# Performance work log

Hardware: AMD Instinct MI355X
Metric: run time of the kernel (lower is better)

## Reference

```python
import jax, jax.numpy as jnp
import numpy as np

K = 3  # kernel_size

def setup_inputs() -> dict:
    key = jax.random.key(0)
    k1, k2, k3 = jax.random.split(key, 3)
    B, T, G, F, O = 4, 512, 129, 96, 96
    x = jax.random.normal(k1, (B, T, G, F), dtype=jnp.float32)
    # kaiming_uniform_(a=sqrt(5)) -> bound = sqrt(6/((1+5)*fan_in)) = 1/sqrt(fan_in), fan_in = F*K
    fan_in = F * K
    wb = 1.0 / np.sqrt(fan_in)
    weight = jax.random.uniform(k2, (G, O, F, K), dtype=jnp.float32, minval=-wb, maxval=wb)
    bias = jax.random.uniform(k3, (G, O), dtype=jnp.float32, minval=-wb, maxval=wb)
    return {"x": x, "weight": weight, "bias": bias}

def reference(x, weight, bias):
    # x: [B, T, G, F]; weight: [G, O, F, K]; bias: [G, O]
    B, T, G, F = x.shape
    pad = K // 2
    xp = jnp.pad(x, ((0, 0), (pad, pad), (0, 0), (0, 0)))  # [B, T+2p, G, F]
    # gather K shifted views -> [B, T, G, F, K] (same windows as unfold with padding K//2)
    xw = jnp.stack([xp[:, k:k + T] for k in range(K)], axis=-1)
    out = jnp.einsum('btgfk,gofk->btgo', xw, weight)
    out = out + bias  # broadcast [G, O] over [B, T, G, O]
    return out
```

## Files before the change

kernel.cpp:

```cpp
#include <hip/hip_runtime.h>

typedef unsigned short ushort_t;
typedef __attribute__((ext_vector_type(8))) short short8;
typedef __attribute__((ext_vector_type(4))) float floatx4;

#define G_   129
#define F_   96
#define O_   96
#define T_   512
#define KD   288
#define LDB  296
#define SROW 40
#define SLAB (36 * SROW)

__device__ __forceinline__ unsigned f2bf(float f) {
    unsigned u = __builtin_bit_cast(unsigned, f);
    u += 0x7FFFu + ((u >> 16) & 1u);
    return u >> 16;
}
__device__ __forceinline__ unsigned pk2(float a, float b) {
    return f2bf(a) | (f2bf(b) << 16);
}

__global__ __launch_bounds__(512, 4) void conv_mfma(
    const float* __restrict__ x, const float* __restrict__ w,
    const float* __restrict__ bias, float* __restrict__ out)
{
    __shared__ __align__(16) ushort_t Wl[O_ * LDB];
    __shared__ __align__(16) ushort_t Xs[8 * SLAB];

    const int g    = blockIdx.y;
    const int m0   = blockIdx.x * 256;
    const int tid  = threadIdx.x;
    const int wave = tid >> 6;
    const int lane = tid & 63;
    const int ln   = lane & 15;
    const int q    = lane >> 4;

    const int m0r = m0 + wave * 32;
    const int b   = m0r >> 9;
    const int tb  = m0r & 511;

    const float* tp[5];
    int  laddr[5];
    bool wr[5], vld[5];
    #pragma unroll
    for (int i = 0; i < 5; ++i) {
        int task = i * 64 + lane;
        int row = task >> 3;
        int seg = task & 7;
        int tl = tb + row - 1;
        wr[i]  = row < 34;
        vld[i] = wr[i] && ((unsigned)tl < (unsigned)T_);
        int tc = tl < 0 ? 0 : (tl > T_ - 1 ? T_ - 1 : tl);
        tp[i] = x + ((size_t)((b * T_ + tc) * G_ + g) * F_ + seg * 4);
        laddr[i] = wave * SLAB + row * SROW + seg * 4;
    }

    auto issueX = [&](int fb, floatx4* v) {
        #pragma unroll
        for (int i = 0; i < 5; ++i)
            v[i] = *(const floatx4*)(tp[i] + fb * 32);
    };
    auto writeX = [&](const floatx4* v) {
        #pragma unroll
        for (int i = 0; i < 5; ++i) {
            if (wr[i]) {
                unsigned lo = pk2(v[i][0], v[i][1]);
                unsigned hi = pk2(v[i][2], v[i][3]);
                if (!vld[i]) { lo = 0u; hi = 0u; }
                uint2 d; d.x = lo; d.y = hi;
                *(uint2*)&Xs[laddr[i]] = d;
            }
        }
    };

    floatx4 va[5], vb[5];
    issueX(0, va);

    {
        const float* wg = w + (size_t)g * (O_ * KD);
        #pragma unroll
        for (int i = 0; i < 5; ++i) {
            int task = i * 512 + tid;
            if (task < 2304) {
                int o = task / 24;
                int u = task - o * 24;
                const float* p = wg + o * KD + u * 12;
                float4 A = *(const float4*)(p);
                float4 B = *(const float4*)(p + 4);
                float4 C = *(const float4*)(p + 8);
                int base = o * LDB + u * 4;
                uint2 d0, d1, d2;
                d0.x = pk2(A.x, A.w);  d0.y = pk2(B.z, C.y);
                d1.x = pk2(A.y, B.x);  d1.y = pk2(B.w, C.z);
                d2.x = pk2(A.z, B.y);  d2.y = pk2(C.x, C.w);
                *(uint2*)&Wl[base]       = d0;
                *(uint2*)&Wl[base +  96] = d1;
                *(uint2*)&Wl[base + 192] = d2;
            }
        }
    }

    float bv[6];
    #pragma unroll
    for (int nt = 0; nt < 6; ++nt) bv[nt] = bias[g * O_ + nt * 16 + ln];

    __syncthreads();

    floatx4 acc[2][6];
    #pragma unroll
    for (int s = 0; s < 2; ++s)
        #pragma unroll
        for (int nt = 0; nt < 6; ++nt)
            acc[s][nt] = (floatx4){0.f, 0.f, 0.f, 0.f};

    auto compute = [&](int fb) {
        #pragma unroll
        for (int kk = 0; kk < 3; ++kk) {
            const short8 a0 = *(const short8*)&Xs[wave * SLAB + (ln + kk) * SROW + q * 8];
            const short8 a1 = *(const short8*)&Xs[wave * SLAB + (16 + ln + kk) * SROW + q * 8];
            const int c32 = (kk * 3 + fb) * 32;
            #pragma unroll
            for (int nt = 0; nt < 6; ++nt) {
                const short8 bbv = *(const short8*)&Wl[(nt * 16 + ln) * LDB + c32 + q * 8];
                acc[0][nt] = __builtin_amdgcn_mfma_f32_16x16x32_bf16(a0, bbv, acc[0][nt], 0, 0, 0);
                acc[1][nt] = __builtin_amdgcn_mfma_f32_16x16x32_bf16(a1, bbv, acc[1][nt], 0, 0, 0);
            }
        }
    };

    issueX(1, vb);
    writeX(va);
    compute(0);
    issueX(2, va);
    writeX(vb);
    compute(1);
    writeX(va);
    compute(2);

    #pragma unroll
    for (int s = 0; s < 2; ++s) {
        int mbase = m0 + wave * 32 + s * 16 + q * 4;
        #pragma unroll
        for (int nt = 0; nt < 6; ++nt) {
            int o = nt * 16 + ln;
            #pragma unroll
            for (int r = 0; r < 4; ++r) {
                int m = mbase + r;
                out[(size_t)(m * G_ + g) * O_ + o] = acc[s][nt][r] + bv[nt];
            }
        }
    }
}

extern "C" void kernel_launch(void* const* d_in, const int* in_sizes, int n_in,
                              void* d_out, int out_size, void* d_ws, size_t ws_size,
                              hipStream_t stream) {
    const float* x    = (const float*)d_in[0];
    const float* w    = (const float*)d_in[1];
    const float* bias = (const float*)d_in[2];
    float* out = (float*)d_out;
    dim3 grid(2048 / 256, G_);
    conv_mfma<<<grid, dim3(512), 0, stream>>>(x, w, bias, out);
}
```

Measured before the change: 214.2 us.

## Process two M-tiles per block, reusing weights and prefetching the next tile's X

Each block now handles two consecutive 256-row tiles for one group, so the converted bf16 weight slab in LDS is loaded once and serves twice as many rows. The grid is flattened to 544 blocks with a swizzle that places 8 adjacent groups in consecutive blocks. All three feature chunks of X are loaded up front, and the second tile's loads are issued before the first tile's last compute and epilogue so they overlap. In exchange the block count drops and register pressure rises from holding three X buffers, which may reduce occupancy. Blocks with group index 129 or higher exit immediately.

```diff
diff --git a/kernel.cpp b/kernel.cpp
--- a/kernel.cpp
+++ b/kernel.cpp
@@ -29,33 +29,44 @@
     __shared__ __align__(16) ushort_t Wl[O_ * LDB];
     __shared__ __align__(16) ushort_t Xs[8 * SLAB];
 
-    const int g    = blockIdx.y;
-    const int m0   = blockIdx.x * 256;
+    const int bid = blockIdx.x;
+    const int c   = bid & 7;
+    const int s   = bid >> 3;
+    const int g   = c + ((s >> 2) << 3);
+    if (g >= G_) return;
+    const int mt  = s & 3;
+    const int m0base = mt * 512;
+
     const int tid  = threadIdx.x;
     const int wave = tid >> 6;
     const int lane = tid & 63;
     const int ln   = lane & 15;
     const int q    = lane >> 4;
 
-    const int m0r = m0 + wave * 32;
-    const int b   = m0r >> 9;
-    const int tb  = m0r & 511;
-
-    const float* tp[5];
-    int  laddr[5];
-    bool wr[5], vld[5];
+    int  laddr[5], rowv[5], segv[5];
+    bool wr[5];
     #pragma unroll
     for (int i = 0; i < 5; ++i) {
         int task = i * 64 + lane;
-        int row = task >> 3;
-        int seg = task & 7;
-        int tl = tb + row - 1;
-        wr[i]  = row < 34;
-        vld[i] = wr[i] && ((unsigned)tl < (unsigned)T_);
-        int tc = tl < 0 ? 0 : (tl > T_ - 1 ? T_ - 1 : tl);
-        tp[i] = x + ((size_t)((b * T_ + tc) * G_ + g) * F_ + seg * 4);
-        laddr[i] = wave * SLAB + row * SROW + seg * 4;
+        rowv[i] = task >> 3;
+        segv[i] = task & 7;
+        wr[i]   = rowv[i] < 34;
+        laddr[i] = wave * SLAB + rowv[i] * SROW + segv[i] * 4;
     }
+
+    const float* tp[5];
+    bool vld[5];
+    auto computeTP = [&](int m0r) {
+        int b  = m0r >> 9;
+        int tb = m0r & 511;
+        #pragma unroll
+        for (int i = 0; i < 5; ++i) {
+            int tl = tb + rowv[i] - 1;
+            vld[i] = wr[i] && ((unsigned)tl < (unsigned)T_);
+            int tc = tl < 0 ? 0 : (tl > T_ - 1 ? T_ - 1 : tl);
+            tp[i] = x + ((size_t)((b * T_ + tc) * G_ + g) * F_ + segv[i] * 4);
+        }
+    };
 
     auto issueX = [&](int fb, floatx4* v) {
         #pragma unroll
@@ -75,8 +86,9 @@
         }
     };
 
-    floatx4 va[5], vb[5];
-    issueX(0, va);
+    floatx4 vA[5], vB[5], vC[5];
+    computeTP(m0base + wave * 32);
+    issueX(0, vA); issueX(1, vB); issueX(2, vC);
 
     {
         const float* wg = w + (size_t)g * (O_ * KD);
@@ -109,11 +121,13 @@
     __syncthreads();
 
     floatx4 acc[2][6];
-    #pragma unroll
-    for (int s = 0; s < 2; ++s)
+    auto zeroAcc = [&]() {
         #pragma unroll
-        for (int nt = 0; nt < 6; ++nt)
-            acc[s][nt] = (floatx4){0.f, 0.f, 0.f, 0.f};
+        for (int s2 = 0; s2 < 2; ++s2)
+            #pragma unroll
+            for (int nt = 0; nt < 6; ++nt)
+                acc[s2][nt] = (floatx4){0.f, 0.f, 0.f, 0.f};
+    };
 
     auto compute = [&](int fb) {
         #pragma unroll
@@ -130,28 +144,37 @@
         }
     };
 
-    issueX(1, vb);
-    writeX(va);
-    compute(0);
-    issueX(2, va);
-    writeX(vb);
-    compute(1);
-    writeX(va);
-    compute(2);
-
-    #pragma unroll
-    for (int s = 0; s < 2; ++s) {
-        int mbase = m0 + wave * 32 + s * 16 + q * 4;
+    auto epilogue = [&](int m0t) {
         #pragma unroll
-        for (int nt = 0; nt < 6; ++nt) {
-            int o = nt * 16 + ln;
+        for (int s2 = 0; s2 < 2; ++s2) {
+            int mbase = m0t + wave * 32 + s2 * 16 + q * 4;
             #pragma unroll
-            for (int r = 0; r < 4; ++r) {
-                int m = mbase + r;
-                out[(size_t)(m * G_ + g) * O_ + o] = acc[s][nt][r] + bv[nt];
+            for (int nt = 0; nt < 6; ++nt) {
+                int o = nt * 16 + ln;
+                #pragma unroll
+                for (int r = 0; r < 4; ++r) {
+                    int m = mbase + r;
+                    out[(size_t)(m * G_ + g) * O_ + o] = acc[s2][nt][r] + bv[nt];
+                }
             }
         }
-    }
+    };
+
+    zeroAcc();
+
+    writeX(vA); compute(0);
+    writeX(vB); compute(1);
+    writeX(vC);
+    computeTP(m0base + 256 + wave * 32);
+    issueX(0, vA); issueX(1, vB); issueX(2, vC);
+    compute(2);
+    epilogue(m0base);
+    zeroAcc();
+
+    writeX(vA); compute(0);
+    writeX(vB); compute(1);
+    writeX(vC); compute(2);
+    epilogue(m0base + 256);
 }
 
 extern "C" void kernel_launch(void* const* d_in, const int* in_sizes, int n_in,
@@ -161,6 +184,5 @@
     const float* w    = (const float*)d_in[1];
     const float* bias = (const float*)d_in[2];
     float* out = (float*)d_out;
-    dim3 grid(2048 / 256, G_);
-    conv_mfma<<<grid, dim3(512), 0, stream>>>(x, w, bias, out);
+    conv_mfma<<<dim3(544), dim3(512), 0, stream>>>(x, w, bias, out);
 }
```

Measured after the change: 224.3 us. +4.7%, slower.

## Split output channels across blocks, remap grid for locality, issue all X loads upfront

Applied to the files above, without the earlier changes.

Each block now computes half of the output channels (48) for a 256-row tile, which halves weight LDS and accumulator registers and doubles the block count. A 1D grid swizzle groups eight consecutive groups per chunk so that concurrently running blocks touch neighbouring x rows. All three X chunk loads are issued before the weight staging, and launch bounds are raised to 6 to fit more blocks per CU. The cost is that every x tile is now loaded and converted twice, once per output half, and some blocks in the padded last chunk exit early.

```diff
diff --git a/kernel.cpp b/kernel.cpp
--- a/kernel.cpp
+++ b/kernel.cpp
@@ -7,6 +7,7 @@
 #define G_   129
 #define F_   96
 #define O_   96
+#define OH_  48
 #define T_   512
 #define KD   288
 #define LDB  296
@@ -22,15 +23,23 @@
     return f2bf(a) | (f2bf(b) << 16);
 }
 
-__global__ __launch_bounds__(512, 4) void conv_mfma(
+__global__ __launch_bounds__(512, 6) void conv_mfma(
     const float* __restrict__ x, const float* __restrict__ w,
     const float* __restrict__ bias, float* __restrict__ out)
 {
-    __shared__ __align__(16) ushort_t Wl[O_ * LDB];
+    __shared__ __align__(16) ushort_t Wl[OH_ * LDB];
     __shared__ __align__(16) ushort_t Xs[8 * SLAB];
 
-    const int g    = blockIdx.y;
-    const int m0   = blockIdx.x * 256;
+    const int bid = blockIdx.x;
+    const int c   = bid & 7;
+    const int s   = bid >> 3;
+    const int g   = c + ((s >> 4) << 3);
+    if (g >= G_) return;
+    const int sub = s & 15;
+    const int mt  = sub >> 1;
+    const int oh  = sub & 1;
+    const int m0  = mt * 256;
+
     const int tid  = threadIdx.x;
     const int wave = tid >> 6;
     const int lane = tid & 63;
@@ -49,7 +58,7 @@
         int task = i * 64 + lane;
         int row = task >> 3;
         int seg = task & 7;
-        int tl = tb + row - 1;
+        int tl  = tb + row - 1;
         wr[i]  = row < 34;
         vld[i] = wr[i] && ((unsigned)tl < (unsigned)T_);
         int tc = tl < 0 ? 0 : (tl > T_ - 1 ? T_ - 1 : tl);
@@ -75,15 +84,15 @@
         }
     };
 
-    floatx4 va[5], vb[5];
-    issueX(0, va);
+    floatx4 vA[5], vB[5], vC[5];
+    issueX(0, vA); issueX(1, vB); issueX(2, vC);
 
     {
-        const float* wg = w + (size_t)g * (O_ * KD);
+        const float* wg = w + ((size_t)g * O_ + oh * OH_) * KD;
         #pragma unroll
-        for (int i = 0; i < 5; ++i) {
+        for (int i = 0; i < 3; ++i) {
             int task = i * 512 + tid;
-            if (task < 2304) {
+            if (task < OH_ * 24) {
                 int o = task / 24;
                 int u = task - o * 24;
                 const float* p = wg + o * KD + u * 12;
@@ -102,18 +111,18 @@
         }
     }
 
-    float bv[6];
+    float bv[3];
     #pragma unroll
-    for (int nt = 0; nt < 6; ++nt) bv[nt] = bias[g * O_ + nt * 16 + ln];
+    for (int nt = 0; nt < 3; ++nt) bv[nt] = bias[g * O_ + oh * OH_ + nt * 16 + ln];
 
     __syncthreads();
 
-    floatx4 acc[2][6];
+    floatx4 acc[2][3];
     #pragma unroll
-    for (int s = 0; s < 2; ++s)
+    for (int s2 = 0; s2 < 2; ++s2)
         #pragma unroll
-        for (int nt = 0; nt < 6; ++nt)
-            acc[s][nt] = (floatx4){0.f, 0.f, 0.f, 0.f};
+        for (int nt = 0; nt < 3; ++nt)
+            acc[s2][nt] = (floatx4){0.f, 0.f, 0.f, 0.f};
 
     auto compute = [&](int fb) {
         #pragma unroll
@@ -122,7 +131,7 @@
             const short8 a1 = *(const short8*)&Xs[wave * SLAB + (16 + ln + kk) * SROW + q * 8];
             const int c32 = (kk * 3 + fb) * 32;
             #pragma unroll
-            for (int nt = 0; nt < 6; ++nt) {
+            for (int nt = 0; nt < 3; ++nt) {
                 const short8 bbv = *(const short8*)&Wl[(nt * 16 + ln) * LDB + c32 + q * 8];
                 acc[0][nt] = __builtin_amdgcn_mfma_f32_16x16x32_bf16(a0, bbv, acc[0][nt], 0, 0, 0);
                 acc[1][nt] = __builtin_amdgcn_mfma_f32_16x16x32_bf16(a1, bbv, acc[1][nt], 0, 0, 0);
@@ -130,25 +139,20 @@
         }
     };
 
-    issueX(1, vb);
-    writeX(va);
-    compute(0);
-    issueX(2, va);
-    writeX(vb);
-    compute(1);
-    writeX(va);
-    compute(2);
+    writeX(vA); compute(0);
+    writeX(vB); compute(1);
+    writeX(vC); compute(2);
 
     #pragma unroll
-    for (int s = 0; s < 2; ++s) {
-        int mbase = m0 + wave * 32 + s * 16 + q * 4;
+    for (int s2 = 0; s2 < 2; ++s2) {
+        int mbase = m0 + wave * 32 + s2 * 16 + q * 4;
         #pragma unroll
-        for (int nt = 0; nt < 6; ++nt) {
-            int o = nt * 16 + ln;
+        for (int nt = 0; nt < 3; ++nt) {
+            int o = oh * OH_ + nt * 16 + ln;
             #pragma unroll
             for (int r = 0; r < 4; ++r) {
                 int m = mbase + r;
-                out[(size_t)(m * G_ + g) * O_ + o] = acc[s][nt][r] + bv[nt];
+                out[(size_t)(m * G_ + g) * O_ + o] = acc[s2][nt][r] + bv[nt];
             }
         }
     }
@@ -161,6 +165,5 @@
     const float* w    = (const float*)d_in[1];
     const float* bias = (const float*)d_in[2];
     float* out = (float*)d_out;
-    dim3 grid(2048 / 256, G_);
-    conv_mfma<<<grid, dim3(512), 0, stream>>>(x, w, bias, out);
+    conv_mfma<<<dim3(2176), dim3(512), 0, stream>>>(x, w, bias, out);
 }
```

Result: slower. 236.2 us (+10.3%).

## Load A fragments directly into registers and remap blocks for group locality

Applied to the files above, without the earlier changes.

Removes the shared-memory staging of the input slab: each lane now loads its MFMA A-fragment rows straight from global memory, converts them with the hardware packed bf16 convert instruction, and zeroes padded rows with a mask. This drops the LDS writes and reads for X, but each row is loaded three times (once per kernel tap), which raises global/L2 traffic and register use. The grid becomes a flat 1D launch whose block-to-(group, m-tile) mapping places 8 consecutive groups together, so neighbouring blocks read adjacent feature columns of the same rows and should share cache lines; a few blocks exit early as padding.

```diff
diff --git a/kernel.cpp b/kernel.cpp
--- a/kernel.cpp
+++ b/kernel.cpp
@@ -3,6 +3,7 @@
 typedef unsigned short ushort_t;
 typedef __attribute__((ext_vector_type(8))) short short8;
 typedef __attribute__((ext_vector_type(4))) float floatx4;
+typedef __attribute__((ext_vector_type(4))) unsigned uintx4;
 
 #define G_   129
 #define F_   96
@@ -10,8 +11,6 @@
 #define T_   512
 #define KD   288
 #define LDB  296
-#define SROW 40
-#define SLAB (36 * SROW)
 
 __device__ __forceinline__ unsigned f2bf(float f) {
     unsigned u = __builtin_bit_cast(unsigned, f);
@@ -21,16 +20,26 @@
 __device__ __forceinline__ unsigned pk2(float a, float b) {
     return f2bf(a) | (f2bf(b) << 16);
 }
+__device__ __forceinline__ unsigned cvtpk(float lo, float hi) {
+    unsigned r;
+    asm("v_cvt_pk_bf16_f32 %0, %1, %2" : "=v"(r) : "v"(lo), "v"(hi));
+    return r;
+}
 
 __global__ __launch_bounds__(512, 4) void conv_mfma(
     const float* __restrict__ x, const float* __restrict__ w,
     const float* __restrict__ bias, float* __restrict__ out)
 {
     __shared__ __align__(16) ushort_t Wl[O_ * LDB];
-    __shared__ __align__(16) ushort_t Xs[8 * SLAB];
 
-    const int g    = blockIdx.y;
-    const int m0   = blockIdx.x * 256;
+    const int bid = blockIdx.x;
+    const int c   = bid & 7;
+    const int s   = bid >> 3;
+    const int g   = c + ((s >> 3) << 3);
+    if (g >= G_) return;
+    const int mt  = s & 7;
+    const int m0  = mt * 256;
+
     const int tid  = threadIdx.x;
     const int wave = tid >> 6;
     const int lane = tid & 63;
@@ -41,42 +50,30 @@
     const int b   = m0r >> 9;
     const int tb  = m0r & 511;
 
-    const float* tp[5];
-    int  laddr[5];
-    bool wr[5], vld[5];
+    const float* pA[2][3];
+    unsigned msk[2][3];
     #pragma unroll
-    for (int i = 0; i < 5; ++i) {
-        int task = i * 64 + lane;
-        int row = task >> 3;
-        int seg = task & 7;
-        int tl = tb + row - 1;
-        wr[i]  = row < 34;
-        vld[i] = wr[i] && ((unsigned)tl < (unsigned)T_);
-        int tc = tl < 0 ? 0 : (tl > T_ - 1 ? T_ - 1 : tl);
-        tp[i] = x + ((size_t)((b * T_ + tc) * G_ + g) * F_ + seg * 4);
-        laddr[i] = wave * SLAB + row * SROW + seg * 4;
-    }
+    for (int s2 = 0; s2 < 2; ++s2)
+        #pragma unroll
+        for (int kk = 0; kk < 3; ++kk) {
+            int t = tb + s2 * 16 + ln + kk - 1;
+            msk[s2][kk] = ((unsigned)t < (unsigned)T_) ? 0xFFFFFFFFu : 0u;
+            int tc = t < 0 ? 0 : (t > T_ - 1 ? T_ - 1 : t);
+            pA[s2][kk] = x + ((size_t)((b * T_ + tc) * G_ + g) * F_ + q * 8);
+        }
 
-    auto issueX = [&](int fb, floatx4* v) {
+    floatx4 u[2][3][2];
+    auto issueA = [&](int fb) {
         #pragma unroll
-        for (int i = 0; i < 5; ++i)
-            v[i] = *(const floatx4*)(tp[i] + fb * 32);
-    };
-    auto writeX = [&](const floatx4* v) {
-        #pragma unroll
-        for (int i = 0; i < 5; ++i) {
-            if (wr[i]) {
-                unsigned lo = pk2(v[i][0], v[i][1]);
-                unsigned hi = pk2(v[i][2], v[i][3]);
-                if (!vld[i]) { lo = 0u; hi = 0u; }
-                uint2 d; d.x = lo; d.y = hi;
-                *(uint2*)&Xs[laddr[i]] = d;
+        for (int s2 = 0; s2 < 2; ++s2)
+            #pragma unroll
+            for (int kk = 0; kk < 3; ++kk) {
+                u[s2][kk][0] = *(const floatx4*)(pA[s2][kk] + fb * 32);
+                u[s2][kk][1] = *(const floatx4*)(pA[s2][kk] + fb * 32 + 4);
             }
-        }
     };
 
-    floatx4 va[5], vb[5];
-    issueX(0, va);
+    issueA(0);
 
     {
         const float* wg = w + (size_t)g * (O_ * KD);
@@ -85,12 +82,12 @@
             int task = i * 512 + tid;
             if (task < 2304) {
                 int o = task / 24;
-                int u = task - o * 24;
-                const float* p = wg + o * KD + u * 12;
+                int uu = task - o * 24;
+                const float* p = wg + o * KD + uu * 12;
                 float4 A = *(const float4*)(p);
                 float4 B = *(const float4*)(p + 4);
                 float4 C = *(const float4*)(p + 8);
-                int base = o * LDB + u * 4;
+                int base = o * LDB + uu * 4;
                 uint2 d0, d1, d2;
                 d0.x = pk2(A.x, A.w);  d0.y = pk2(B.z, C.y);
                 d1.x = pk2(A.y, B.x);  d1.y = pk2(B.w, C.z);
@@ -110,45 +107,53 @@
 
     floatx4 acc[2][6];
     #pragma unroll
-    for (int s = 0; s < 2; ++s)
+    for (int s2 = 0; s2 < 2; ++s2)
         #pragma unroll
         for (int nt = 0; nt < 6; ++nt)
-            acc[s][nt] = (floatx4){0.f, 0.f, 0.f, 0.f};
+            acc[s2][nt] = (floatx4){0.f, 0.f, 0.f, 0.f};
 
-    auto compute = [&](int fb) {
+    short8 a[2][3];
+    auto packA = [&]() {
+        #pragma unroll
+        for (int s2 = 0; s2 < 2; ++s2)
+            #pragma unroll
+            for (int kk = 0; kk < 3; ++kk) {
+                unsigned mk = msk[s2][kk];
+                uintx4 d;
+                d[0] = cvtpk(u[s2][kk][0][0], u[s2][kk][0][1]) & mk;
+                d[1] = cvtpk(u[s2][kk][0][2], u[s2][kk][0][3]) & mk;
+                d[2] = cvtpk(u[s2][kk][1][0], u[s2][kk][1][1]) & mk;
+                d[3] = cvtpk(u[s2][kk][1][2], u[s2][kk][1][3]) & mk;
+                a[s2][kk] = __builtin_bit_cast(short8, d);
+            }
+    };
+
+    #pragma unroll
+    for (int fb = 0; fb < 3; ++fb) {
+        packA();
+        if (fb < 2) issueA(fb + 1);
         #pragma unroll
         for (int kk = 0; kk < 3; ++kk) {
-            const short8 a0 = *(const short8*)&Xs[wave * SLAB + (ln + kk) * SROW + q * 8];
-            const short8 a1 = *(const short8*)&Xs[wave * SLAB + (16 + ln + kk) * SROW + q * 8];
             const int c32 = (kk * 3 + fb) * 32;
             #pragma unroll
             for (int nt = 0; nt < 6; ++nt) {
                 const short8 bbv = *(const short8*)&Wl[(nt * 16 + ln) * LDB + c32 + q * 8];
-                acc[0][nt] = __builtin_amdgcn_mfma_f32_16x16x32_bf16(a0, bbv, acc[0][nt], 0, 0, 0);
-                acc[1][nt] = __builtin_amdgcn_mfma_f32_16x16x32_bf16(a1, bbv, acc[1][nt], 0, 0, 0);
+                acc[0][nt] = __builtin_amdgcn_mfma_f32_16x16x32_bf16(a[0][kk], bbv, acc[0][nt], 0, 0, 0);
+                acc[1][nt] = __builtin_amdgcn_mfma_f32_16x16x32_bf16(a[1][kk], bbv, acc[1][nt], 0, 0, 0);
             }
         }
-    };
-
-    issueX(1, vb);
-    writeX(va);
-    compute(0);
-    issueX(2, va);
-    writeX(vb);
-    compute(1);
-    writeX(va);
-    compute(2);
+    }
 
     #pragma unroll
-    for (int s = 0; s < 2; ++s) {
-        int mbase = m0 + wave * 32 + s * 16 + q * 4;
+    for (int s2 = 0; s2 < 2; ++s2) {
+        int mbase = m0 + wave * 32 + s2 * 16 + q * 4;
         #pragma unroll
         for (int nt = 0; nt < 6; ++nt) {
             int o = nt * 16 + ln;
             #pragma unroll
             for (int r = 0; r < 4; ++r) {
                 int m = mbase + r;
-                out[(size_t)(m * G_ + g) * O_ + o] = acc[s][nt][r] + bv[nt];
+                out[(size_t)(m * G_ + g) * O_ + o] = acc[s2][nt][r] + bv[nt];
             }
         }
     }
@@ -161,6 +166,5 @@
     const float* w    = (const float*)d_in[1];
     const float* bias = (const float*)d_in[2];
     float* out = (float*)d_out;
-    dim3 grid(2048 / 256, G_);
-    conv_mfma<<<grid, dim3(512), 0, stream>>>(x, w, bias, out);
+    conv_mfma<<<dim3(1088), dim3(512), 0, stream>>>(x, w, bias, out);
 }
```

Measured after the change: 245.1 us. 1.14x slower.
